# Kernel optimization log

Hardware: AMD Instinct MI355X
Metric: run time of the kernel (lower is better)

Reference implementation:

```python
import jax, jax.numpy as jnp
import numpy as np

NOOBJECT_SCALE = 1.0
OBJECT_SCALE = 5.0
SIL_THRESH = 0.6
COORD_SCALE = 1.0
CLASS_SCALE = 1.0
SEEN = 0
MAX_GT = 50


def _iou_cxcywh(a, b):
    # a, b: [..., 4] boxes as (cx, cy, w, h); matches bbox_ious(x1y1x2y2=False)
    ax1 = a[..., 0] - a[..., 2] * 0.5; ax2 = a[..., 0] + a[..., 2] * 0.5
    ay1 = a[..., 1] - a[..., 3] * 0.5; ay2 = a[..., 1] + a[..., 3] * 0.5
    bx1 = b[..., 0] - b[..., 2] * 0.5; bx2 = b[..., 0] + b[..., 2] * 0.5
    by1 = b[..., 1] - b[..., 3] * 0.5; by2 = b[..., 1] + b[..., 3] * 0.5
    iw = jnp.maximum(jnp.minimum(ax2, bx2) - jnp.maximum(ax1, bx1), 0.0)
    ih = jnp.maximum(jnp.minimum(ay2, by2) - jnp.maximum(ay1, by1), 0.0)
    inter = iw * ih
    union = a[..., 2] * a[..., 3] + b[..., 2] * b[..., 3] - inter
    return jnp.where(union > 0, inter / union, 0.0)


def _forward(output, target, anchors):
    nB, ch, nH, nW = output.shape
    nA = anchors.shape[0] // 2
    nC = ch // nA - 5
    anc = anchors.reshape(nA, 2)
    out = output.reshape(nB, nA, 5 + nC, nH, nW)
    x = jax.nn.sigmoid(out[:, :, 0])
    y = jax.nn.sigmoid(out[:, :, 1])
    w = out[:, :, 2]
    h = out[:, :, 3]
    conf = jax.nn.sigmoid(out[:, :, 4])
    cls_logits = jnp.transpose(out[:, :, 5:], (0, 1, 3, 4, 2))  # [B,A,H,W,C]

    sg = jax.lax.stop_gradient
    f32 = jnp.float32
    grid_x = jnp.arange(nW, dtype=f32)[None, None, None, :]
    grid_y = jnp.arange(nH, dtype=f32)[None, None, :, None]
    aw = anc[:, 0][None, :, None, None]
    ah = anc[:, 1][None, :, None, None]
    # decoded pred boxes are computed on detached data in the torch code
    pred = sg(jnp.stack([x + grid_x, y + grid_y, jnp.exp(w) * aw, jnp.exp(h) * ah], axis=-1))  # [B,A,H,W,4]

    # ---- build_targets (vectorized) ----
    t = sg(target).reshape(nB, MAX_GT, 5)
    anc_c = sg(anc)
    gx = t[:, :, 1] * nW; gy = t[:, :, 2] * nH
    gw = t[:, :, 3] * nW; gh = t[:, :, 4] * nH
    valid = t[:, :, 1] > 0  # loop breaks at first x==0; zeros only trail valid boxes

    total = nB * nA * nH * nW
    pred_flat = pred.reshape(nB, nA * nH * nW, 4)
    gt_boxes = jnp.stack([gx, gy, gw, gh], axis=-1)  # [B,50,4]
    ious = _iou_cxcywh(pred_flat[:, None], gt_boxes[:, :, None])  # [B,50,AHW]
    cur_ious = jnp.max(jnp.where(valid[:, :, None], ious, 0.0), axis=1)  # [B,AHW]
    conf_mask = jnp.where(cur_ious > SIL_THRESH, 0.0, NOOBJECT_SCALE).reshape(total)

    if SEEN < 12800:
        coord_mask = jnp.ones(total, f32)
        tx = jnp.full(total, 0.5, f32)
        ty = jnp.full(total, 0.5, f32)
    else:
        coord_mask = jnp.zeros(total, f32)
        tx = jnp.zeros(total, f32)
        ty = jnp.zeros(total, f32)
    tw = jnp.zeros(total, f32); th = jnp.zeros(total, f32)
    tconf = jnp.zeros(total, f32)
    cls_mask = jnp.zeros(total, f32)
    tcls = jnp.zeros(total, jnp.int32)

    # anchor matching: IoU of (0,0,aw,ah) vs (0,0,gw,gh)
    z = jnp.zeros_like(gw)
    gt_wh = jnp.stack([z, z, gw, gh], axis=-1)  # [B,50,4]
    anc_boxes = jnp.concatenate([jnp.zeros((nA, 2), f32), anc_c], axis=1)  # [A,4]
    a_ious = _iou_cxcywh(anc_boxes[None, None], gt_wh[:, :, None])  # [B,50,A]
    best_n = jnp.argmax(a_ious, axis=-1)  # first max == strict '>' loop semantics

    gi = jnp.clip(gx.astype(jnp.int32), 0, nW - 1)
    gj = jnp.clip(gy.astype(jnp.int32), 0, nH - 1)
    b_idx = jnp.arange(nB)[:, None]
    flat = ((b_idx * nA + best_n) * nH + gj) * nW + gi  # [B,50]
    safe = jnp.where(valid, flat, total)  # OOB -> dropped by scatter

    aw_b = anc_c[best_n, 0]; ah_b = anc_c[best_n, 1]
    eps = 1e-12
    twv = jnp.where(valid, jnp.log(jnp.maximum(gw, eps) / aw_b), 0.0)
    thv = jnp.where(valid, jnp.log(jnp.maximum(gh, eps) / ah_b), 0.0)
    pbest = pred.reshape(total, 4)[jnp.clip(flat, 0, total - 1)]  # [B,50,4]
    iou_best = _iou_cxcywh(pbest, gt_boxes)  # [B,50]

    coord_mask = coord_mask.at[safe].set(1.0, mode='drop')
    cls_mask = cls_mask.at[safe].set(1.0, mode='drop')
    conf_mask = conf_mask.at[safe].set(OBJECT_SCALE, mode='drop')
    tx = tx.at[safe].set(gx - gi.astype(f32), mode='drop')
    ty = ty.at[safe].set(gy - gj.astype(f32), mode='drop')
    tw = tw.at[safe].set(twv, mode='drop')
    th = th.at[safe].set(thv, mode='drop')
    tconf = tconf.at[safe].set(iou_best, mode='drop')
    tcls = tcls.at[safe].set(t[:, :, 0].astype(jnp.int32), mode='drop')

    shp = (nB, nA, nH, nW)
    cm = coord_mask.reshape(shp)
    cfm = jnp.sqrt(conf_mask.reshape(shp))
    txr = tx.reshape(shp); tyr = ty.reshape(shp)
    twr = tw.reshape(shp); thr = th.reshape(shp)
    tconf_r = tconf.reshape(shp)
    clsm = cls_mask.reshape(shp)
    tcls_r = tcls.reshape(shp)

    loss_x = COORD_SCALE * jnp.sum((x * cm - txr * cm) ** 2) / 2.0
    loss_y = COORD_SCALE * jnp.sum((y * cm - tyr * cm) ** 2) / 2.0
    loss_w = COORD_SCALE * jnp.sum((w * cm - twr * cm) ** 2) / 2.0
    loss_h = COORD_SCALE * jnp.sum((h * cm - thr * cm) ** 2) / 2.0
    loss_conf = jnp.sum((conf * cfm - tconf_r * cfm) ** 2) / 2.0
    logp = jax.nn.log_softmax(cls_logits, axis=-1)
    nll = -jnp.take_along_axis(logp, tcls_r[..., None], axis=-1)[..., 0]
    loss_cls = CLASS_SCALE * jnp.sum(nll * clsm)
    return loss_x + loss_y + loss_w + loss_h + loss_conf + loss_cls


def setup_inputs() -> dict:
    key = jax.random.key(0)
    nB, nA, nC, nH, nW = 16, 5, 20, 64, 64
    output = jax.random.normal(key, (nB, nA * (5 + nC), nH, nW), jnp.float32) * 0.5
    anchors = jnp.array([1.3221, 1.73145, 3.19275, 4.00944, 5.05587,
                         8.09892, 9.47112, 4.84053, 11.2364, 10.0071], jnp.float32)
    rng = np.random.default_rng(0)
    nGT = 10
    tgt = np.zeros((nB, MAX_GT, 5), np.float32)
    tgt[:, :nGT, 0] = rng.integers(0, nC, (nB, nGT))
    tgt[:, :nGT, 1] = rng.uniform(0.05, 0.95, (nB, nGT))
    tgt[:, :nGT, 2] = rng.uniform(0.05, 0.95, (nB, nGT))
    tgt[:, :nGT, 3] = rng.uniform(0.02, 0.30, (nB, nGT))
    tgt[:, :nGT, 4] = rng.uniform(0.02, 0.30, (nB, nGT))
    target = jnp.asarray(tgt.reshape(nB, MAX_GT * 5))
    return {"output": output, "target": target, "anchors": anchors}


def reference(output, target, anchors):
    return _forward(output, target, anchors)
```

## Files before the change

kernel.cpp:

```cpp
#include <hip/hip_runtime.h>
#include <math.h>

#define NB 16
#define NA 5
#define NC 20
#define NH 64
#define NW 64
#define MAXGT 50
#define NGT (NB * MAXGT)
#define CELLS (NH * NW)
#define CH (NA * (5 + NC))
#define TOTAL (NB * NA * NH * NW)
#define SIL_THRESH 0.6f
#define OBJECT_SCALE 5.0f

__device__ __forceinline__ float sigmoidf_(float v) {
    return 1.0f / (1.0f + __expf(-v));
}

__global__ __launch_bounds__(256) void gt_prep(
    const float* __restrict__ out, const float* __restrict__ tgt,
    const float* __restrict__ anc, float* __restrict__ ws_f,
    int* __restrict__ ws_i, float* __restrict__ d_out)
{
    int g = blockIdx.x * blockDim.x + threadIdx.x;
    if (g == 0) d_out[0] = 0.0f;
    if (g >= NGT) return;

    int b = g / MAXGT;
    const float* t = tgt + (size_t)g * 5;
    float cls = t[0], xn = t[1], yn = t[2], wn = t[3], hn = t[4];
    bool valid = xn > 0.0f;
    float gx = xn * NW, gy = yn * NH, gw = wn * NW, gh = hn * NH;

    int bn = 0; float best = -1.0f;
    for (int a = 0; a < NA; ++a) {
        float aw = anc[2 * a], ah = anc[2 * a + 1];
        float inter = fminf(aw, gw) * fminf(ah, gh);
        float uni = aw * ah + gw * gh - inter;
        float iou = uni > 0.0f ? inter / uni : 0.0f;
        if (iou > best) { best = iou; bn = a; }
    }
    float aw = anc[2 * bn], ah = anc[2 * bn + 1];
    int gi = (int)gx; gi = gi < 0 ? 0 : (gi > NW - 1 ? NW - 1 : gi);
    int gj = (int)gy; gj = gj < 0 ? 0 : (gj > NH - 1 ? NH - 1 : gj);
    int flat = ((b * NA + bn) * NH + gj) * NW + gi;

    int cell = gj * NW + gi;
    const float* base = out + ((size_t)b * CH + bn * 25) * CELLS + cell;
    float xr = base[0];
    float yr = base[CELLS];
    float wr = base[2 * CELLS];
    float hr = base[3 * CELLS];
    float px = sigmoidf_(xr) + (float)gi;
    float py = sigmoidf_(yr) + (float)gj;
    float pw = __expf(wr) * aw;
    float ph = __expf(hr) * ah;

    float ax1 = px - pw * 0.5f, ax2 = px + pw * 0.5f;
    float ay1 = py - ph * 0.5f, ay2 = py + ph * 0.5f;
    float bx1 = gx - gw * 0.5f, bx2 = gx + gw * 0.5f;
    float by1 = gy - gh * 0.5f, by2 = gy + gh * 0.5f;
    float iw = fmaxf(fminf(ax2, bx2) - fmaxf(ax1, bx1), 0.0f);
    float ih = fmaxf(fminf(ay2, by2) - fmaxf(ay1, by1), 0.0f);
    float inter = iw * ih;
    float uni = pw * ph + gw * gh - inter;
    float iou = uni > 0.0f ? inter / uni : 0.0f;

    ws_f[0 * NGT + g] = bx1;
    ws_f[1 * NGT + g] = bx2;
    ws_f[2 * NGT + g] = by1;
    ws_f[3 * NGT + g] = by2;
    ws_f[4 * NGT + g] = gw * gh;
    ws_f[5 * NGT + g] = gx - (float)gi;
    ws_f[6 * NGT + g] = gy - (float)gj;
    ws_f[7 * NGT + g] = __logf(fmaxf(gw, 1e-12f) / aw);
    ws_f[8 * NGT + g] = __logf(fmaxf(gh, 1e-12f) / ah);
    ws_f[9 * NGT + g] = iou;
    ws_i[0 * NGT + g] = valid ? flat : -1;
    ws_i[1 * NGT + g] = (int)cls;
}

__global__ __launch_bounds__(256) void yolo_loss(
    const float* __restrict__ out, const float* __restrict__ anc,
    const float* __restrict__ ws_f, const int* __restrict__ ws_i,
    float* __restrict__ d_out)
{
    __shared__ float s_bx1[MAXGT], s_bx2[MAXGT], s_by1[MAXGT], s_by2[MAXGT];
    __shared__ float s_area[MAXGT], s_tx[MAXGT], s_ty[MAXGT], s_tw[MAXGT];
    __shared__ float s_th[MAXGT], s_tc[MAXGT];
    __shared__ int s_flat[MAXGT], s_cls[MAXGT];

    int idx = blockIdx.x * 256 + threadIdx.x;
    int b = idx / (NA * CELLS);

    if (threadIdx.x < MAXGT) {
        int g = b * MAXGT + threadIdx.x;
        s_bx1[threadIdx.x]  = ws_f[0 * NGT + g];
        s_bx2[threadIdx.x]  = ws_f[1 * NGT + g];
        s_by1[threadIdx.x]  = ws_f[2 * NGT + g];
        s_by2[threadIdx.x]  = ws_f[3 * NGT + g];
        s_area[threadIdx.x] = ws_f[4 * NGT + g];
        s_tx[threadIdx.x]   = ws_f[5 * NGT + g];
        s_ty[threadIdx.x]   = ws_f[6 * NGT + g];
        s_tw[threadIdx.x]   = ws_f[7 * NGT + g];
        s_th[threadIdx.x]   = ws_f[8 * NGT + g];
        s_tc[threadIdx.x]   = ws_f[9 * NGT + g];
        s_flat[threadIdx.x] = ws_i[0 * NGT + g];
        s_cls[threadIdx.x]  = ws_i[1 * NGT + g];
    }
    __syncthreads();

    int r = idx - b * NA * CELLS;
    int a = r / CELLS;
    int cell = r - a * CELLS;
    int j = cell / NW, i = cell - j * NW;

    const float* base = out + ((size_t)b * CH + a * 25) * CELLS + cell;
    float xr = base[0];
    float yr = base[CELLS];
    float wr = base[2 * CELLS];
    float hr = base[3 * CELLS];
    float cr = base[4 * CELLS];

    float sx = sigmoidf_(xr), sy = sigmoidf_(yr), sc = sigmoidf_(cr);
    float aw = anc[2 * a], ah = anc[2 * a + 1];
    float pw = __expf(wr) * aw, ph = __expf(hr) * ah;
    float px = sx + (float)i, py = sy + (float)j;
    float ax1 = px - pw * 0.5f, ax2 = px + pw * 0.5f;
    float ay1 = py - ph * 0.5f, ay2 = py + ph * 0.5f;
    float parea = pw * ph;

    float maxiou = 0.0f;
    int match = -1;
    #pragma unroll 10
    for (int g = 0; g < MAXGT; ++g) {
        int fg = s_flat[g];
        if (fg < 0) continue;
        float iw = fmaxf(fminf(ax2, s_bx2[g]) - fmaxf(ax1, s_bx1[g]), 0.0f);
        float ih = fmaxf(fminf(ay2, s_by2[g]) - fmaxf(ay1, s_by1[g]), 0.0f);
        float inter = iw * ih;
        float uni = parea + s_area[g] - inter;
        float iou = uni > 0.0f ? inter / uni : 0.0f;
        maxiou = fmaxf(maxiou, iou);
        if (fg == idx) match = g;
    }

    float tx = 0.5f, ty = 0.5f, tw = 0.0f, th = 0.0f, tconf = 0.0f;
    float cscale = (maxiou > SIL_THRESH) ? 0.0f : 1.0f;
    float loss = 0.0f;

    if (match >= 0) {
        tx = s_tx[match]; ty = s_ty[match];
        tw = s_tw[match]; th = s_th[match];
        tconf = s_tc[match]; cscale = OBJECT_SCALE;
        const float* cl = base + 5 * CELLS;
        float lg[NC];
        float mx = -1e30f;
        #pragma unroll
        for (int c = 0; c < NC; ++c) { lg[c] = cl[c * CELLS]; mx = fmaxf(mx, lg[c]); }
        float se = 0.0f;
        #pragma unroll
        for (int c = 0; c < NC; ++c) se += __expf(lg[c] - mx);
        float lse = mx + __logf(se);
        loss += lse - lg[s_cls[match]];
    }

    float dx = sx - tx, dy = sy - ty, dw = wr - tw, dh = hr - th, dc = sc - tconf;
    loss += 0.5f * (dx * dx + dy * dy + dw * dw + dh * dh)
          + 0.5f * cscale * dc * dc;

    float v = loss;
    #pragma unroll
    for (int off = 32; off > 0; off >>= 1) v += __shfl_down(v, off, 64);
    __shared__ float ssum[4];
    int lane = threadIdx.x & 63, wv = threadIdx.x >> 6;
    if (lane == 0) ssum[wv] = v;
    __syncthreads();
    if (threadIdx.x == 0)
        atomicAdd(d_out, ssum[0] + ssum[1] + ssum[2] + ssum[3]);
}

extern "C" void kernel_launch(void* const* d_in, const int* in_sizes, int n_in,
                              void* d_out, int out_size, void* d_ws, size_t ws_size,
                              hipStream_t stream) {
    const float* out = (const float*)d_in[0];
    const float* tgt = (const float*)d_in[1];
    const float* anc = (const float*)d_in[2];
    float* ws_f = (float*)d_ws;
    int*   ws_i = (int*)((char*)d_ws + (size_t)10 * NGT * sizeof(float));
    float* o = (float*)d_out;

    gt_prep<<<(NGT + 255) / 256, 256, 0, stream>>>(out, tgt, anc, ws_f, ws_i, o);
    yolo_loss<<<TOTAL / 256, 256, 0, stream>>>(out, anc, ws_f, ws_i, o);
}
```

Before: 96.68 us.

## Process two cells per thread and replace IoU division with threshold test

```diff
diff --git a/kernel.cpp b/kernel.cpp
--- a/kernel.cpp
+++ b/kernel.cpp
@@ -11,17 +11,22 @@
 #define CELLS (NH * NW)
 #define CH (NA * (5 + NC))
 #define TOTAL (NB * NA * NH * NW)
-#define SIL_THRESH 0.6f
 #define OBJECT_SCALE 5.0f
 
-__device__ __forceinline__ float sigmoidf_(float v) {
-    return 1.0f / (1.0f + __expf(-v));
+#define WS_BOX_OFF  0
+#define WS_EPI_OFF  12800
+#define WS_THR_OFF  38400
+#define WS_FLAT_OFF 41600
+
+__device__ __forceinline__ float fast_sigmoid(float v) {
+    return __builtin_amdgcn_rcpf(1.0f + __expf(-v));
 }
 
 __global__ __launch_bounds__(256) void gt_prep(
     const float* __restrict__ out, const float* __restrict__ tgt,
-    const float* __restrict__ anc, float* __restrict__ ws_f,
-    int* __restrict__ ws_i, float* __restrict__ d_out)
+    const float* __restrict__ anc, float4* __restrict__ ws_box,
+    float4* __restrict__ ws_epi, float* __restrict__ ws_thr,
+    int* __restrict__ ws_flat, float* __restrict__ d_out)
 {
     int g = blockIdx.x * blockDim.x + threadIdx.x;
     if (g == 0) d_out[0] = 0.0f;
@@ -52,132 +57,172 @@
     float yr = base[CELLS];
     float wr = base[2 * CELLS];
     float hr = base[3 * CELLS];
-    float px = sigmoidf_(xr) + (float)gi;
-    float py = sigmoidf_(yr) + (float)gj;
+    float px = fast_sigmoid(xr) + (float)gi;
+    float py = fast_sigmoid(yr) + (float)gj;
     float pw = __expf(wr) * aw;
     float ph = __expf(hr) * ah;
 
+    float bx1 = gx - gw * 0.5f, bx2 = gx + gw * 0.5f;
+    float by1 = gy - gh * 0.5f, by2 = gy + gh * 0.5f;
     float ax1 = px - pw * 0.5f, ax2 = px + pw * 0.5f;
     float ay1 = py - ph * 0.5f, ay2 = py + ph * 0.5f;
-    float bx1 = gx - gw * 0.5f, bx2 = gx + gw * 0.5f;
-    float by1 = gy - gh * 0.5f, by2 = gy + gh * 0.5f;
     float iw = fmaxf(fminf(ax2, bx2) - fmaxf(ax1, bx1), 0.0f);
     float ih = fmaxf(fminf(ay2, by2) - fmaxf(ay1, by1), 0.0f);
     float inter = iw * ih;
     float uni = pw * ph + gw * gh - inter;
     float iou = uni > 0.0f ? inter / uni : 0.0f;
 
-    ws_f[0 * NGT + g] = bx1;
-    ws_f[1 * NGT + g] = bx2;
-    ws_f[2 * NGT + g] = by1;
-    ws_f[3 * NGT + g] = by2;
-    ws_f[4 * NGT + g] = gw * gh;
-    ws_f[5 * NGT + g] = gx - (float)gi;
-    ws_f[6 * NGT + g] = gy - (float)gj;
-    ws_f[7 * NGT + g] = __logf(fmaxf(gw, 1e-12f) / aw);
-    ws_f[8 * NGT + g] = __logf(fmaxf(gh, 1e-12f) / ah);
-    ws_f[9 * NGT + g] = iou;
-    ws_i[0 * NGT + g] = valid ? flat : -1;
-    ws_i[1 * NGT + g] = (int)cls;
+    if (valid) {
+        ws_box[g] = make_float4(bx1, bx2, by1, by2);
+        ws_thr[g] = 0.375f * (gw * gh);
+        ws_flat[g] = flat;
+    } else {
+        ws_box[g] = make_float4(3e18f, -3e18f, 3e18f, -3e18f);
+        ws_thr[g] = 3e18f;
+        ws_flat[g] = -1;
+    }
+    ws_epi[2 * g]     = make_float4(gx - (float)gi, gy - (float)gj,
+                                    __logf(fmaxf(gw, 1e-12f) / aw),
+                                    __logf(fmaxf(gh, 1e-12f) / ah));
+    ws_epi[2 * g + 1] = make_float4(iou, cls, 0.0f, 0.0f);
 }
 
 __global__ __launch_bounds__(256) void yolo_loss(
     const float* __restrict__ out, const float* __restrict__ anc,
-    const float* __restrict__ ws_f, const int* __restrict__ ws_i,
+    const float4* __restrict__ ws_box, const float4* __restrict__ ws_epi,
+    const float* __restrict__ ws_thr, const int* __restrict__ ws_flat,
     float* __restrict__ d_out)
 {
-    __shared__ float s_bx1[MAXGT], s_bx2[MAXGT], s_by1[MAXGT], s_by2[MAXGT];
-    __shared__ float s_area[MAXGT], s_tx[MAXGT], s_ty[MAXGT], s_tw[MAXGT];
-    __shared__ float s_th[MAXGT], s_tc[MAXGT];
-    __shared__ int s_flat[MAXGT], s_cls[MAXGT];
-
-    int idx = blockIdx.x * 256 + threadIdx.x;
-    int b = idx / (NA * CELLS);
-
-    if (threadIdx.x < MAXGT) {
-        int g = b * MAXGT + threadIdx.x;
-        s_bx1[threadIdx.x]  = ws_f[0 * NGT + g];
-        s_bx2[threadIdx.x]  = ws_f[1 * NGT + g];
-        s_by1[threadIdx.x]  = ws_f[2 * NGT + g];
-        s_by2[threadIdx.x]  = ws_f[3 * NGT + g];
-        s_area[threadIdx.x] = ws_f[4 * NGT + g];
-        s_tx[threadIdx.x]   = ws_f[5 * NGT + g];
-        s_ty[threadIdx.x]   = ws_f[6 * NGT + g];
-        s_tw[threadIdx.x]   = ws_f[7 * NGT + g];
-        s_th[threadIdx.x]   = ws_f[8 * NGT + g];
-        s_tc[threadIdx.x]   = ws_f[9 * NGT + g];
-        s_flat[threadIdx.x] = ws_i[0 * NGT + g];
-        s_cls[threadIdx.x]  = ws_i[1 * NGT + g];
+    __shared__ float4 s_box[MAXGT];
+    __shared__ float  s_thr[MAXGT];
+    __shared__ int    s_flat[MAXGT];
+    __shared__ float  ssum[4];
+
+    int tid = threadIdx.x;
+    int b = blockIdx.x / 40;
+
+    if (tid < MAXGT) {
+        int g = b * MAXGT + tid;
+        s_box[tid]  = ws_box[g];
+        s_thr[tid]  = ws_thr[g];
+        s_flat[tid] = ws_flat[g];
     }
     __syncthreads();
 
-    int r = idx - b * NA * CELLS;
-    int a = r / CELLS;
-    int cell = r - a * CELLS;
-    int j = cell / NW, i = cell - j * NW;
-
-    const float* base = out + ((size_t)b * CH + a * 25) * CELLS + cell;
-    float xr = base[0];
-    float yr = base[CELLS];
-    float wr = base[2 * CELLS];
-    float hr = base[3 * CELLS];
-    float cr = base[4 * CELLS];
-
-    float sx = sigmoidf_(xr), sy = sigmoidf_(yr), sc = sigmoidf_(cr);
+    int q = blockIdx.x * 256 + tid;
+    int id0 = 2 * q;
+    int r = id0 - b * (NA * CELLS);
+    int a = r >> 12;
+    int cell = r & (CELLS - 1);
+    int j = cell >> 6, i = cell & 63;
+
+    const float* base = out + (((size_t)(b * CH + a * 25)) << 12) + cell;
+    float2 xr = *(const float2*)(base);
+    float2 yr = *(const float2*)(base + CELLS);
+    float2 wr = *(const float2*)(base + 2 * CELLS);
+    float2 hr = *(const float2*)(base + 3 * CELLS);
+    float2 cr = *(const float2*)(base + 4 * CELLS);
+
     float aw = anc[2 * a], ah = anc[2 * a + 1];
-    float pw = __expf(wr) * aw, ph = __expf(hr) * ah;
-    float px = sx + (float)i, py = sy + (float)j;
-    float ax1 = px - pw * 0.5f, ax2 = px + pw * 0.5f;
-    float ay1 = py - ph * 0.5f, ay2 = py + ph * 0.5f;
-    float parea = pw * ph;
-
-    float maxiou = 0.0f;
-    int match = -1;
+
+    float sx0 = fast_sigmoid(xr.x), sx1 = fast_sigmoid(xr.y);
+    float sy0 = fast_sigmoid(yr.x), sy1 = fast_sigmoid(yr.y);
+    float pw0 = __expf(wr.x) * aw,  pw1 = __expf(wr.y) * aw;
+    float ph0 = __expf(hr.x) * ah,  ph1 = __expf(hr.y) * ah;
+    float px0 = sx0 + (float)i,     px1 = sx1 + (float)(i + 1);
+    float py0 = sy0 + (float)j,     py1 = sy1 + (float)j;
+
+    float ax1_0 = px0 - pw0 * 0.5f, ax2_0 = px0 + pw0 * 0.5f;
+    float ay1_0 = py0 - ph0 * 0.5f, ay2_0 = py0 + ph0 * 0.5f;
+    float ax1_1 = px1 - pw1 * 0.5f, ax2_1 = px1 + pw1 * 0.5f;
+    float ay1_1 = py1 - ph1 * 0.5f, ay2_1 = py1 + ph1 * 0.5f;
+    float pthr0 = 0.375f * (pw0 * ph0);
+    float pthr1 = 0.375f * (pw1 * ph1);
+
+    float sil0 = -1.0f, sil1 = -1.0f;
+    int m0 = -1, m1 = -1;
+
     #pragma unroll 10
     for (int g = 0; g < MAXGT; ++g) {
+        float4 B = s_box[g];
+        float tg = s_thr[g];
         int fg = s_flat[g];
-        if (fg < 0) continue;
-        float iw = fmaxf(fminf(ax2, s_bx2[g]) - fmaxf(ax1, s_bx1[g]), 0.0f);
-        float ih = fmaxf(fminf(ay2, s_by2[g]) - fmaxf(ay1, s_by1[g]), 0.0f);
-        float inter = iw * ih;
-        float uni = parea + s_area[g] - inter;
-        float iou = uni > 0.0f ? inter / uni : 0.0f;
-        maxiou = fmaxf(maxiou, iou);
-        if (fg == idx) match = g;
-    }
-
-    float tx = 0.5f, ty = 0.5f, tw = 0.0f, th = 0.0f, tconf = 0.0f;
-    float cscale = (maxiou > SIL_THRESH) ? 0.0f : 1.0f;
+
+        float iw0 = fminf(ax2_0, B.y) - fmaxf(ax1_0, B.x);
+        float ih0 = fminf(ay2_0, B.w) - fmaxf(ay1_0, B.z);
+        float in0 = fmaxf(iw0, 0.0f) * fmaxf(ih0, 0.0f);
+        sil0 = fmaxf(sil0, in0 - (pthr0 + tg));
+
+        float iw1 = fminf(ax2_1, B.y) - fmaxf(ax1_1, B.x);
+        float ih1 = fminf(ay2_1, B.w) - fmaxf(ay1_1, B.z);
+        float in1 = fmaxf(iw1, 0.0f) * fmaxf(ih1, 0.0f);
+        sil1 = fmaxf(sil1, in1 - (pthr1 + tg));
+
+        m0 = (fg == id0)     ? g : m0;
+        m1 = (fg == id0 + 1) ? g : m1;
+    }
+
+    float sc0 = fast_sigmoid(cr.x), sc1 = fast_sigmoid(cr.y);
     float loss = 0.0f;
 
-    if (match >= 0) {
-        tx = s_tx[match]; ty = s_ty[match];
-        tw = s_tw[match]; th = s_th[match];
-        tconf = s_tc[match]; cscale = OBJECT_SCALE;
-        const float* cl = base + 5 * CELLS;
-        float lg[NC];
-        float mx = -1e30f;
-        #pragma unroll
-        for (int c = 0; c < NC; ++c) { lg[c] = cl[c * CELLS]; mx = fmaxf(mx, lg[c]); }
-        float se = 0.0f;
-        #pragma unroll
-        for (int c = 0; c < NC; ++c) se += __expf(lg[c] - mx);
-        float lse = mx + __logf(se);
-        loss += lse - lg[s_cls[match]];
-    }
-
-    float dx = sx - tx, dy = sy - ty, dw = wr - tw, dh = hr - th, dc = sc - tconf;
-    loss += 0.5f * (dx * dx + dy * dy + dw * dw + dh * dh)
-          + 0.5f * cscale * dc * dc;
+    {
+        float tx = 0.5f, ty = 0.5f, tw = 0.0f, th = 0.0f, tc = 0.0f;
+        float cs = (sil0 > 0.0f) ? 0.0f : 1.0f;
+        if (m0 >= 0) {
+            int g = b * MAXGT + m0;
+            float4 e0 = ws_epi[2 * g], e1 = ws_epi[2 * g + 1];
+            tx = e0.x; ty = e0.y; tw = e0.z; th = e0.w;
+            tc = e1.x; cs = OBJECT_SCALE;
+            int cls = (int)e1.y;
+            const float* cl = base + 5 * CELLS;
+            float mx = -1e30f;
+            #pragma unroll
+            for (int c = 0; c < NC; ++c) mx = fmaxf(mx, cl[c * CELLS]);
+            float se = 0.0f, lt = 0.0f;
+            #pragma unroll
+            for (int c = 0; c < NC; ++c) {
+                float v = cl[c * CELLS];
+                se += __expf(v - mx);
+                if (c == cls) lt = v;
+            }
+            loss += mx + __logf(se) - lt;
+        }
+        float dx = sx0 - tx, dy = sy0 - ty, dw = wr.x - tw, dh = hr.x - th, dc = sc0 - tc;
+        loss += 0.5f * (dx * dx + dy * dy + dw * dw + dh * dh) + 0.5f * cs * dc * dc;
+    }
+    {
+        float tx = 0.5f, ty = 0.5f, tw = 0.0f, th = 0.0f, tc = 0.0f;
+        float cs = (sil1 > 0.0f) ? 0.0f : 1.0f;
+        if (m1 >= 0) {
+            int g = b * MAXGT + m1;
+            float4 e0 = ws_epi[2 * g], e1 = ws_epi[2 * g + 1];
+            tx = e0.x; ty = e0.y; tw = e0.z; th = e0.w;
+            tc = e1.x; cs = OBJECT_SCALE;
+            int cls = (int)e1.y;
+            const float* cl = base + 1 + 5 * CELLS;
+            float mx = -1e30f;
+            #pragma unroll
+            for (int c = 0; c < NC; ++c) mx = fmaxf(mx, cl[c * CELLS]);
+            float se = 0.0f, lt = 0.0f;
+            #pragma unroll
+            for (int c = 0; c < NC; ++c) {
+                float v = cl[c * CELLS];
+                se += __expf(v - mx);
+                if (c == cls) lt = v;
+            }
+            loss += mx + __logf(se) - lt;
+        }
+        float dx = sx1 - tx, dy = sy1 - ty, dw = wr.y - tw, dh = hr.y - th, dc = sc1 - tc;
+        loss += 0.5f * (dx * dx + dy * dy + dw * dw + dh * dh) + 0.5f * cs * dc * dc;
+    }
 
     float v = loss;
     #pragma unroll
     for (int off = 32; off > 0; off >>= 1) v += __shfl_down(v, off, 64);
-    __shared__ float ssum[4];
-    int lane = threadIdx.x & 63, wv = threadIdx.x >> 6;
+    int lane = tid & 63, wv = tid >> 6;
     if (lane == 0) ssum[wv] = v;
     __syncthreads();
-    if (threadIdx.x == 0)
+    if (tid == 0)
         atomicAdd(d_out, ssum[0] + ssum[1] + ssum[2] + ssum[3]);
 }
 
@@ -187,10 +232,15 @@
     const float* out = (const float*)d_in[0];
     const float* tgt = (const float*)d_in[1];
     const float* anc = (const float*)d_in[2];
-    float* ws_f = (float*)d_ws;
-    int*   ws_i = (int*)((char*)d_ws + (size_t)10 * NGT * sizeof(float));
+    char* ws = (char*)d_ws;
+    float4* ws_box = (float4*)(ws + WS_BOX_OFF);
+    float4* ws_epi = (float4*)(ws + WS_EPI_OFF);
+    float* ws_thr = (float*)(ws + WS_THR_OFF);
+    int* ws_flat = (int*)(ws + WS_FLAT_OFF);
     float* o = (float*)d_out;
 
-    gt_prep<<<(NGT + 255) / 256, 256, 0, stream>>>(out, tgt, anc, ws_f, ws_i, o);
-    yolo_loss<<<TOTAL / 256, 256, 0, stream>>>(out, anc, ws_f, ws_i, o);
-}
+    gt_prep<<<(NGT + 255) / 256, 256, 0, stream>>>(out, tgt, anc, ws_box, ws_epi,
+                                                   ws_thr, ws_flat, o);
+    yolo_loss<<<(TOTAL / 2) / 256, 256, 0, stream>>>(out, anc, ws_box, ws_epi,
+                                                     ws_thr, ws_flat, o);
+}
```

Result: faster. 88.61 us (-8.4%).
